# Performance work log

Hardware: AMD Instinct MI355X
Metric: run time of the kernel (lower is better)

The kernel has to match this reference:

```python
import jax, jax.numpy as jnp
import numpy as np


def setup_inputs() -> dict:
    key = jax.random.key(0)
    ks = jax.random.split(key, 4)
    B, L, E = 2, 2048, 512
    scale = 0.02
    return {
        "x": jax.random.normal(ks[0], (B, L, E), dtype=jnp.float32),
        "Wq": jax.random.normal(ks[1], (E, E), dtype=jnp.float32) * scale,
        "bq": jnp.zeros((E,), dtype=jnp.float32),
        "Wk": jax.random.normal(ks[2], (E, E), dtype=jnp.float32) * scale,
        "bk": jnp.zeros((E,), dtype=jnp.float32),
        "Wv": jax.random.normal(ks[3], (E, E), dtype=jnp.float32) * scale,
        "bv": jnp.zeros((E,), dtype=jnp.float32),
        "window_size": 64,
    }


def reference(x, Wq, bq, Wk, bk, Wv, bv, window_size):
    # x: [B, L, E]; Linear weights stored torch-style as [out, in].
    B, L, E = x.shape
    q = jnp.einsum("ble,fe->blf", x, Wq) + bq  # [B, L, E]
    k = jnp.einsum("ble,fe->blf", x, Wk) + bk
    v = jnp.einsum("ble,fe->blf", x, Wv) + bv

    w = window_size
    W = 2 * w + 1
    # Window indices per query position i: [i-w, i+w], clipped; invalid masked.
    offsets = jnp.arange(-w, w + 1)                 # [W]
    idx = jnp.arange(L)[:, None] + offsets[None, :]  # [L, W]
    valid = (idx >= 0) & (idx < L)                   # [L, W]
    idx_c = jnp.clip(idx, 0, L - 1)

    k_win = k[:, idx_c]  # [B, L, W, E]
    v_win = v[:, idx_c]  # [B, L, W, E]

    scores = jnp.einsum("ble,blwe->blw", q, k_win) / jnp.sqrt(jnp.float32(E))
    scores = jnp.where(valid[None, :, :], scores, -jnp.inf)
    probs = jax.nn.softmax(scores, axis=-1)          # [B, L, W]
    out = jnp.einsum("blw,blwe->ble", probs, v_win)  # [B, L, E]
    return out
```

## Files before the change

### kernel.cpp

```cpp
#include <hip/hip_runtime.h>
#include <cstdint>
#include <cstddef>

#define L_SEQ 2048
#define E_DIM 512
#define B_SZ 2
#define WIN 64
#define SCALE_QK 0.044194173824159216f

typedef __attribute__((ext_vector_type(8))) short short8;
typedef __attribute__((ext_vector_type(4))) float floatx4;

__device__ __forceinline__ unsigned short f2bf(float f) {
    unsigned int u = __float_as_uint(f);
    u += 0x7FFFu + ((u >> 16) & 1u);
    return (unsigned short)(u >> 16);
}

__global__ __launch_bounds__(256) void cvt_kernel(
    const float* __restrict__ x, const float* __restrict__ wq,
    const float* __restrict__ wk, const float* __restrict__ wv,
    unsigned short* __restrict__ xb, unsigned short* __restrict__ wb)
{
    long i = (long)blockIdx.x * 256 + threadIdx.x;
    const float* src;
    unsigned short* dst;
    long off;
    if (i < 524288) {
        src = x; dst = xb; off = i;
    } else {
        long j = i - 524288;
        int w = (int)(j >> 16);
        off = j & 65535;
        src = (w == 0) ? wq : ((w == 1) ? wk : wv);
        dst = wb + (long)w * 262144;
    }
    float4 f = ((const float4*)src)[off];
    ushort4 o;
    o.x = f2bf(f.x); o.y = f2bf(f.y); o.z = f2bf(f.z); o.w = f2bf(f.w);
    ((ushort4*)dst)[off] = o;
}

#define ALD 72
__global__ __launch_bounds__(256) void qkv_gemm(
    const unsigned short* __restrict__ xb,
    const unsigned short* __restrict__ wb,
    const float* __restrict__ bq, const float* __restrict__ bk, const float* __restrict__ bv,
    unsigned short* __restrict__ q, unsigned short* __restrict__ k,
    unsigned short* __restrict__ vt)
{
    __shared__ __align__(16) unsigned short As[64 * ALD];
    __shared__ __align__(16) unsigned short Bs[64 * ALD];

    const int t = threadIdx.x;
    const int w = t >> 6, l = t & 63;
    const int m0 = blockIdx.x * 64, n0 = blockIdx.y * 64, z = blockIdx.z;
    const unsigned short* W = wb + (size_t)z * 262144;
    const float* bias = (z == 0) ? bq : ((z == 1) ? bk : bv);

    floatx4 acc[2][2] = {};
    const int wm = (w >> 1) * 32, wn = (w & 1) * 32;
    const int fr = l & 15, fq = l >> 4, fk = fq * 8;

    const int srow = t >> 2, scol = (t & 3) * 16;
    const unsigned short* gA = xb + (size_t)(m0 + srow) * 512 + scol;
    const unsigned short* gB = W  + (size_t)(n0 + srow) * 512 + scol;

    uint4 ra0 = *(const uint4*)(gA);     uint4 ra1 = *(const uint4*)(gA + 8);
    uint4 rb0 = *(const uint4*)(gB);     uint4 rb1 = *(const uint4*)(gB + 8);

    for (int it = 0; it < 8; it++) {
        *(uint4*)&As[srow * ALD + scol]     = ra0;
        *(uint4*)&As[srow * ALD + scol + 8] = ra1;
        *(uint4*)&Bs[srow * ALD + scol]     = rb0;
        *(uint4*)&Bs[srow * ALD + scol + 8] = rb1;
        __syncthreads();
        if (it < 7) {
            int kk = (it + 1) * 64;
            ra0 = *(const uint4*)(gA + kk); ra1 = *(const uint4*)(gA + kk + 8);
            rb0 = *(const uint4*)(gB + kk); rb1 = *(const uint4*)(gB + kk + 8);
        }
        short8 a[2][2], bf[2][2];
#pragma unroll
        for (int i = 0; i < 2; i++)
#pragma unroll
            for (int kh = 0; kh < 2; kh++)
                a[i][kh] = *(const short8*)&As[(wm + i * 16 + fr) * ALD + kh * 32 + fk];
#pragma unroll
        for (int j = 0; j < 2; j++)
#pragma unroll
            for (int kh = 0; kh < 2; kh++)
                bf[j][kh] = *(const short8*)&Bs[(wn + j * 16 + fr) * ALD + kh * 32 + fk];
#pragma unroll
        for (int kh = 0; kh < 2; kh++)
#pragma unroll
            for (int i = 0; i < 2; i++)
#pragma unroll
                for (int j = 0; j < 2; j++)
                    acc[i][j] = __builtin_amdgcn_mfma_f32_16x16x32_bf16(a[i][kh], bf[j][kh], acc[i][j], 0, 0, 0);
        __syncthreads();
    }

    unsigned short* Tl = As;
    float bv_[2];
#pragma unroll
    for (int j = 0; j < 2; j++) bv_[j] = bias[n0 + wn + j * 16 + fr];

    if (z < 2) {
#pragma unroll
        for (int i = 0; i < 2; i++)
#pragma unroll
            for (int j = 0; j < 2; j++)
#pragma unroll
                for (int r = 0; r < 4; r++)
                    Tl[(wm + i * 16 + fq * 4 + r) * ALD + wn + j * 16 + fr] =
                        f2bf(acc[i][j][r] + bv_[j]);
    } else {
#pragma unroll
        for (int i = 0; i < 2; i++)
#pragma unroll
            for (int j = 0; j < 2; j++)
#pragma unroll
                for (int r = 0; r < 4; r++)
                    Tl[(wn + j * 16 + fr) * ALD + wm + i * 16 + fq * 4 + r] =
                        f2bf(acc[i][j][r] + bv_[j]);
    }
    __syncthreads();

    const int tr = t >> 2, tc = (t & 3) * 16;
    uint4 v0 = *(const uint4*)&Tl[tr * ALD + tc];
    uint4 v1 = *(const uint4*)&Tl[tr * ALD + tc + 8];
    if (z < 2) {
        unsigned short* out = (z == 0) ? q : k;
        *(uint4*)&out[(size_t)(m0 + tr) * 512 + n0 + tc]     = v0;
        *(uint4*)&out[(size_t)(m0 + tr) * 512 + n0 + tc + 8] = v1;
    } else {
        *(uint4*)&vt[(size_t)(n0 + tr) * 4096 + m0 + tc]     = v0;
        *(uint4*)&vt[(size_t)(n0 + tr) * 4096 + m0 + tc + 8] = v1;
    }
}

#define SLD 164
__global__ __launch_bounds__(512) void attn_fused(
    const unsigned short* __restrict__ qb, const unsigned short* __restrict__ kb,
    const unsigned short* __restrict__ vt, float* __restrict__ out)
{
    __shared__ __align__(16) float Sl[16 * SLD];

    const int t = threadIdx.x;
    const int w = t >> 6, l = t & 63;
    const int fr = l & 15, fq = l >> 4;
    const int Q0 = blockIdx.x * 16;
    const int b  = blockIdx.y;
    const int R0 = Q0 - WIN;

    {
        const unsigned short* qrow = qb + (size_t)(b * L_SEQ + Q0 + fr) * 512 + fq * 8;
        short8 qf[16];
#pragma unroll
        for (int ks = 0; ks < 16; ks++) qf[ks] = *(const short8*)(qrow + ks * 32);

        for (int nt = w; nt < 9; nt += 8) {
            const int tok = R0 + nt * 16 + fr;
            const bool kvalid = (tok >= 0) && (tok < L_SEQ);
            const int tokc = min(max(tok, 0), L_SEQ - 1);
            const unsigned short* krow = kb + (size_t)(b * L_SEQ + tokc) * 512 + fq * 8;

            floatx4 acc0 = {}, acc1 = {};
            short8 bfr[8];
#pragma unroll
            for (int ks = 0; ks < 8; ks++) bfr[ks] = *(const short8*)(krow + ks * 32);
#pragma unroll
            for (int ks = 0; ks < 8; ks++)
                acc0 = __builtin_amdgcn_mfma_f32_16x16x32_bf16(qf[ks], bfr[ks], acc0, 0, 0, 0);
#pragma unroll
            for (int ks = 0; ks < 8; ks++) bfr[ks] = *(const short8*)(krow + (8 + ks) * 32);
#pragma unroll
            for (int ks = 0; ks < 8; ks++)
                acc1 = __builtin_amdgcn_mfma_f32_16x16x32_bf16(qf[8 + ks], bfr[ks], acc1, 0, 0, 0);

            const int jg = nt * 16 + fr;
#pragma unroll
            for (int r = 0; r < 4; r++) {
                int qq = fq * 4 + r;
                bool valid = kvalid && (jg >= qq) && (jg <= qq + 128);
                Sl[qq * SLD + jg] = valid ? (acc0[r] + acc1[r]) * SCALE_QK : -1e30f;
            }
        }
    }
    __syncthreads();

    const float* Srow = &Sl[fr * SLD + fq * 8];
    float sv[5][8];
#pragma unroll
    for (int ks = 0; ks < 5; ks++) {
        float4 u0 = *(const float4*)(Srow + ks * 32);
        float4 u1 = *(const float4*)(Srow + ks * 32 + 4);
        sv[ks][0] = u0.x; sv[ks][1] = u0.y; sv[ks][2] = u0.z; sv[ks][3] = u0.w;
        sv[ks][4] = u1.x; sv[ks][5] = u1.y; sv[ks][6] = u1.z; sv[ks][7] = u1.w;
    }
    if (fq >= 2) {
#pragma unroll
        for (int j = 0; j < 8; j++) sv[4][j] = -1e30f;
    }
    float m = -1e30f;
#pragma unroll
    for (int ks = 0; ks < 5; ks++)
#pragma unroll
        for (int j = 0; j < 8; j++) m = fmaxf(m, sv[ks][j]);
    m = fmaxf(m, __shfl_xor(m, 16));
    m = fmaxf(m, __shfl_xor(m, 32));
    float sum = 0.f;
#pragma unroll
    for (int ks = 0; ks < 5; ks++)
#pragma unroll
        for (int j = 0; j < 8; j++) { float e = __expf(sv[ks][j] - m); sv[ks][j] = e; sum += e; }
    sum += __shfl_xor(sum, 16);
    sum += __shfl_xor(sum, 32);
    float inv = 1.f / sum;

    short8 a[5];
#pragma unroll
    for (int ks = 0; ks < 5; ks++)
#pragma unroll
        for (int j = 0; j < 8; j++) a[ks][j] = (short)f2bf(sv[ks][j] * inv);

    const int EC = w * 64;
    int tkc[5];
#pragma unroll
    for (int ks = 0; ks < 5; ks++) {
        int tok0 = R0 + ks * 32 + fq * 8;
        tkc[ks] = min(max(tok0, 0), L_SEQ - 8);
    }
    floatx4 oa[4] = {};
#pragma unroll
    for (int et = 0; et < 4; et++) {
        const unsigned short* vrow = vt + (size_t)(EC + et * 16 + fr) * 4096 + b * L_SEQ;
        short8 vfr[5];
#pragma unroll
        for (int ks = 0; ks < 5; ks++) vfr[ks] = *(const short8*)(vrow + tkc[ks]);
#pragma unroll
        for (int ks = 0; ks < 5; ks++)
            oa[et] = __builtin_amdgcn_mfma_f32_16x16x32_bf16(a[ks], vfr[ks], oa[et], 0, 0, 0);
    }

    float* op = out + (size_t)b * L_SEQ * E_DIM;
#pragma unroll
    for (int et = 0; et < 4; et++)
#pragma unroll
        for (int r = 0; r < 4; r++)
            op[(size_t)(Q0 + fq * 4 + r) * 512 + EC + et * 16 + fr] = oa[et][r];
}

extern "C" void kernel_launch(void* const* d_in, const int* in_sizes, int n_in,
                              void* d_out, int out_size, void* d_ws, size_t ws_size,
                              hipStream_t stream)
{
    const float* x  = (const float*)d_in[0];
    const float* Wq = (const float*)d_in[1];
    const float* bq = (const float*)d_in[2];
    const float* Wk = (const float*)d_in[3];
    const float* bk = (const float*)d_in[4];
    const float* Wv = (const float*)d_in[5];
    const float* bv = (const float*)d_in[6];
    float* out = (float*)d_out;

    char* ws = (char*)d_ws;
    unsigned short* qb = (unsigned short*)(ws);
    unsigned short* kb = (unsigned short*)(ws + 4194304);
    unsigned short* vt = (unsigned short*)(ws + 8388608);
    unsigned short* xb = (unsigned short*)(ws + 12582912);
    unsigned short* wb = (unsigned short*)(ws + 16777216);

    cvt_kernel<<<2816, 256, 0, stream>>>(x, Wq, Wk, Wv, xb, wb);
    qkv_gemm<<<dim3(64, 8, 3), 256, 0, stream>>>(xb, wb, bq, bk, bv, qb, kb, vt);
    attn_fused<<<dim3(128, 2), 512, 0, stream>>>(qb, kb, vt, out);
}
```

Before: 106.2 us.

## Enlarge QKV GEMM tiles to 128x128 with direct global-to-LDS swizzled loads

The QKV projection GEMM moves from 64x64 to 128x128 output tiles, with each wave computing a 64x64 sub-tile of 4x4 MFMA fragments. Tiles are now loaded with global_load_lds straight into an XOR-swizzled LDS layout instead of passing through registers into a padded layout. The epilogue writes the tile in two halves through LDS. This raises operand reuse and removes register staging, but the grid shrinks to 384 blocks and the register prefetch overlap of the next k-tile is gone.

```diff
diff --git a/kernel.cpp b/kernel.cpp
--- a/kernel.cpp
+++ b/kernel.cpp
@@ -15,6 +15,13 @@
     unsigned int u = __float_as_uint(f);
     u += 0x7FFFu + ((u >> 16) & 1u);
     return (unsigned short)(u >> 16);
+}
+
+__device__ __forceinline__ void gload_lds16(const void* g, void* l) {
+    __builtin_amdgcn_global_load_lds(
+        (const __attribute__((address_space(1))) unsigned int*)g,
+        (__attribute__((address_space(3))) unsigned int*)l,
+        16, 0, 0);
 }
 
 __global__ __launch_bounds__(256) void cvt_kernel(
@@ -41,7 +48,6 @@
     ((ushort4*)dst)[off] = o;
 }
 
-#define ALD 72
 __global__ __launch_bounds__(256) void qkv_gemm(
     const unsigned short* __restrict__ xb,
     const unsigned short* __restrict__ wb,
@@ -49,94 +55,122 @@
     unsigned short* __restrict__ q, unsigned short* __restrict__ k,
     unsigned short* __restrict__ vt)
 {
-    __shared__ __align__(16) unsigned short As[64 * ALD];
-    __shared__ __align__(16) unsigned short Bs[64 * ALD];
+    __shared__ __align__(16) char lds_raw[32768];
+    unsigned short* As = (unsigned short*)lds_raw;
+    unsigned short* Bs = As + 8192;
 
     const int t = threadIdx.x;
     const int w = t >> 6, l = t & 63;
-    const int m0 = blockIdx.x * 64, n0 = blockIdx.y * 64, z = blockIdx.z;
+    const int m0 = blockIdx.x * 128, n0 = blockIdx.y * 128, z = blockIdx.z;
     const unsigned short* W = wb + (size_t)z * 262144;
     const float* bias = (z == 0) ? bq : ((z == 1) ? bk : bv);
 
-    floatx4 acc[2][2] = {};
-    const int wm = (w >> 1) * 32, wn = (w & 1) * 32;
-    const int fr = l & 15, fq = l >> 4, fk = fq * 8;
-
-    const int srow = t >> 2, scol = (t & 3) * 16;
-    const unsigned short* gA = xb + (size_t)(m0 + srow) * 512 + scol;
-    const unsigned short* gB = W  + (size_t)(n0 + srow) * 512 + scol;
-
-    uint4 ra0 = *(const uint4*)(gA);     uint4 ra1 = *(const uint4*)(gA + 8);
-    uint4 rb0 = *(const uint4*)(gB);     uint4 rb1 = *(const uint4*)(gB + 8);
-
-    for (int it = 0; it < 8; it++) {
-        *(uint4*)&As[srow * ALD + scol]     = ra0;
-        *(uint4*)&As[srow * ALD + scol + 8] = ra1;
-        *(uint4*)&Bs[srow * ALD + scol]     = rb0;
-        *(uint4*)&Bs[srow * ALD + scol + 8] = rb1;
+    const int wr = w >> 1, wc = w & 1;
+    const int fr = l & 15, fq = l >> 4;
+
+    int arow[4], acolb[4];
+#pragma unroll
+    for (int j = 0; j < 4; j++) {
+        int L = (w * 4 + j) * 1024 + l * 16;
+        int row = L >> 7;
+        arow[j]  = row;
+        acolb[j] = (L & 127) ^ ((row & 7) << 4);
+    }
+    const char* gA = (const char*)(xb + (size_t)m0 * 512);
+    const char* gB = (const char*)(W  + (size_t)n0 * 512);
+
+    float bv_[4];
+#pragma unroll
+    for (int j = 0; j < 4; j++) bv_[j] = bias[n0 + wc * 64 + j * 16 + fr];
+
+    floatx4 acc[4][4] = {};
+
+    for (int kt = 0; kt < 8; kt++) {
+#pragma unroll
+        for (int j = 0; j < 4; j++) {
+            gload_lds16(gA + (size_t)arow[j] * 1024 + kt * 128 + acolb[j],
+                        (char*)As + (w * 4 + j) * 1024 + l * 16);
+            gload_lds16(gB + (size_t)arow[j] * 1024 + kt * 128 + acolb[j],
+                        (char*)Bs + (w * 4 + j) * 1024 + l * 16);
+        }
         __syncthreads();
-        if (it < 7) {
-            int kk = (it + 1) * 64;
-            ra0 = *(const uint4*)(gA + kk); ra1 = *(const uint4*)(gA + kk + 8);
-            rb0 = *(const uint4*)(gB + kk); rb1 = *(const uint4*)(gB + kk + 8);
+
+        short8 a[4][2], bfr[4][2];
+#pragma unroll
+        for (int i = 0; i < 4; i++)
+#pragma unroll
+            for (int kh = 0; kh < 2; kh++) {
+                int row = wr * 64 + i * 16 + fr;
+                int cb  = (kh * 64 + fq * 16) ^ ((row & 7) << 4);
+                a[i][kh] = *(const short8*)((const char*)As + (row << 7) + cb);
+            }
+#pragma unroll
+        for (int j = 0; j < 4; j++)
+#pragma unroll
+            for (int kh = 0; kh < 2; kh++) {
+                int row = wc * 64 + j * 16 + fr;
+                int cb  = (kh * 64 + fq * 16) ^ ((row & 7) << 4);
+                bfr[j][kh] = *(const short8*)((const char*)Bs + (row << 7) + cb);
+            }
+#pragma unroll
+        for (int kh = 0; kh < 2; kh++)
+#pragma unroll
+            for (int i = 0; i < 4; i++)
+#pragma unroll
+                for (int j = 0; j < 4; j++)
+                    acc[i][j] = __builtin_amdgcn_mfma_f32_16x16x32_bf16(a[i][kh], bfr[j][kh], acc[i][j], 0, 0, 0);
+        __syncthreads();
+    }
+
+#define TLD 136
+    unsigned short* T = (unsigned short*)lds_raw;
+    const int tr = t >> 2, tc = (t & 3) * 32;
+
+    for (int h = 0; h < 2; h++) {
+        if (h) __syncthreads();
+        if (z < 2) {
+            if (wr == h) {
+#pragma unroll
+                for (int i = 0; i < 4; i++)
+#pragma unroll
+                    for (int j = 0; j < 4; j++)
+#pragma unroll
+                        for (int r = 0; r < 4; r++)
+                            T[(i * 16 + fq * 4 + r) * TLD + wc * 64 + j * 16 + fr] =
+                                f2bf(acc[i][j][r] + bv_[j]);
+            }
+        } else {
+            if (wc == h) {
+#pragma unroll
+                for (int i = 0; i < 4; i++)
+#pragma unroll
+                    for (int j = 0; j < 4; j++)
+#pragma unroll
+                        for (int r = 0; r < 4; r++)
+                            T[(j * 16 + fr) * TLD + wr * 64 + i * 16 + fq * 4 + r] =
+                                f2bf(acc[i][j][r] + bv_[j]);
+            }
         }
-        short8 a[2][2], bf[2][2];
-#pragma unroll
-        for (int i = 0; i < 2; i++)
-#pragma unroll
-            for (int kh = 0; kh < 2; kh++)
-                a[i][kh] = *(const short8*)&As[(wm + i * 16 + fr) * ALD + kh * 32 + fk];
-#pragma unroll
-        for (int j = 0; j < 2; j++)
-#pragma unroll
-            for (int kh = 0; kh < 2; kh++)
-                bf[j][kh] = *(const short8*)&Bs[(wn + j * 16 + fr) * ALD + kh * 32 + fk];
-#pragma unroll
-        for (int kh = 0; kh < 2; kh++)
-#pragma unroll
-            for (int i = 0; i < 2; i++)
-#pragma unroll
-                for (int j = 0; j < 2; j++)
-                    acc[i][j] = __builtin_amdgcn_mfma_f32_16x16x32_bf16(a[i][kh], bf[j][kh], acc[i][j], 0, 0, 0);
         __syncthreads();
-    }
-
-    unsigned short* Tl = As;
-    float bv_[2];
-#pragma unroll
-    for (int j = 0; j < 2; j++) bv_[j] = bias[n0 + wn + j * 16 + fr];
-
-    if (z < 2) {
-#pragma unroll
-        for (int i = 0; i < 2; i++)
-#pragma unroll
-            for (int j = 0; j < 2; j++)
-#pragma unroll
-                for (int r = 0; r < 4; r++)
-                    Tl[(wm + i * 16 + fq * 4 + r) * ALD + wn + j * 16 + fr] =
-                        f2bf(acc[i][j][r] + bv_[j]);
-    } else {
-#pragma unroll
-        for (int i = 0; i < 2; i++)
-#pragma unroll
-            for (int j = 0; j < 2; j++)
-#pragma unroll
-                for (int r = 0; r < 4; r++)
-                    Tl[(wn + j * 16 + fr) * ALD + wm + i * 16 + fq * 4 + r] =
-                        f2bf(acc[i][j][r] + bv_[j]);
-    }
-    __syncthreads();
-
-    const int tr = t >> 2, tc = (t & 3) * 16;
-    uint4 v0 = *(const uint4*)&Tl[tr * ALD + tc];
-    uint4 v1 = *(const uint4*)&Tl[tr * ALD + tc + 8];
-    if (z < 2) {
-        unsigned short* out = (z == 0) ? q : k;
-        *(uint4*)&out[(size_t)(m0 + tr) * 512 + n0 + tc]     = v0;
-        *(uint4*)&out[(size_t)(m0 + tr) * 512 + n0 + tc + 8] = v1;
-    } else {
-        *(uint4*)&vt[(size_t)(n0 + tr) * 4096 + m0 + tc]     = v0;
-        *(uint4*)&vt[(size_t)(n0 + tr) * 4096 + m0 + tc + 8] = v1;
+
+        uint4 u0 = *(const uint4*)&T[tr * TLD + tc];
+        uint4 u1 = *(const uint4*)&T[tr * TLD + tc + 8];
+        uint4 u2 = *(const uint4*)&T[tr * TLD + tc + 16];
+        uint4 u3 = *(const uint4*)&T[tr * TLD + tc + 24];
+        if (z < 2) {
+            unsigned short* out = (z == 0) ? q : k;
+            size_t o = (size_t)(m0 + h * 64 + tr) * 512 + n0 + tc;
+            *(uint4*)&out[o]      = u0;
+            *(uint4*)&out[o + 8]  = u1;
+            *(uint4*)&out[o + 16] = u2;
+            *(uint4*)&out[o + 24] = u3;
+        } else {
+            size_t o = (size_t)(n0 + h * 64 + tr) * 4096 + m0 + tc;
+            *(uint4*)&vt[o]      = u0;
+            *(uint4*)&vt[o + 8]  = u1;
+            *(uint4*)&vt[o + 16] = u2;
+            *(uint4*)&vt[o + 24] = u3;
+        }
     }
 }
 
@@ -273,6 +307,6 @@
     unsigned short* wb = (unsigned short*)(ws + 16777216);
 
     cvt_kernel<<<2816, 256, 0, stream>>>(x, Wq, Wk, Wv, xb, wb);
-    qkv_gemm<<<dim3(64, 8, 3), 256, 0, stream>>>(xb, wb, bq, bk, bv, qb, kb, vt);
+    qkv_gemm<<<dim3(32, 4, 3), 256, 0, stream>>>(xb, wb, bq, bk, bv, qb, kb, vt);
     attn_fused<<<dim3(128, 2), 512, 0, stream>>>(qb, kb, vt, out);
 }
```

New measurement: 106.5 us. Within noise of the previous version (+0.3%).
